# Performance work log

Hardware: AMD Instinct MI355X
Metric: run time of the kernel (lower is better)

## Reference

```python
import jax, jax.numpy as jnp
import numpy as np

E, D, H, K, N = 8, 512, 2048, 2, 1024  # experts, d_model, d_hidden, top_k, tokens
EPS = 1e-5


def _moe_linear(x, idx, W, b):
    # x: (M, in); idx: (M,) expert id per row; W: (E, out, in); b: (E, out)
    # Brute-force: compute per-expert dense GEMMs, select via one-hot (matches
    # BruteForceMoELinear math: y[i] = x[i] @ W[idx[i]].T + b[idx[i]]).
    m = jax.nn.one_hot(idx, W.shape[0], dtype=x.dtype)  # (M, E)
    y = jnp.einsum('me,eoi,mi->mo', m, W, x)
    return y + jnp.take(b, idx, axis=0)


def _forward(inp, gate_w, gate_b, w1, b1, w2, b2, ln_w, ln_b):
    # NaiveGate: linear -> top_k -> softmax over top-k logits
    logits = inp @ gate_w.T + gate_b              # (N, E)
    top_val, top_idx = jax.lax.top_k(logits, K)   # (N, K)
    score = jax.nn.softmax(top_val, axis=-1)      # (N, K)
    # repeat_interleave tokens, dispatch to experts
    x = jnp.repeat(inp, K, axis=0)                # (N*K, D)
    idx = top_idx.reshape(-1)                     # (N*K,)
    x = _moe_linear(x, idx, w1, b1)               # (N*K, H)
    x = jax.nn.gelu(x, approximate=False)         # torch F.gelu default = erf
    x = _moe_linear(x, idx, w2, b2)               # (N*K, D)
    x = x.reshape(N, K, D)
    x = jnp.einsum('nk,nkd->nd', score, x)        # bmm((N,1,K),(N,K,D)) combine
    # post layer norm (pre_lnorm=False)
    mu = jnp.mean(x, axis=-1, keepdims=True)
    var = jnp.var(x, axis=-1, keepdims=True)
    return (x - mu) * jax.lax.rsqrt(var + EPS) * ln_w + ln_b


def setup_inputs() -> dict:
    key = jax.random.key(0)
    ks = jax.random.split(key, 8)
    s = 0.02
    return {
        'inp': jax.random.normal(ks[0], (N, D), dtype=jnp.float32),
        'gate_w': s * jax.random.normal(ks[1], (E, D), dtype=jnp.float32),
        'gate_b': jnp.zeros((E,), dtype=jnp.float32),
        'w1': s * jax.random.normal(ks[2], (E, H, D), dtype=jnp.float32),
        'b1': jnp.zeros((E, H), dtype=jnp.float32),
        'w2': s * jax.random.normal(ks[3], (E, D, H), dtype=jnp.float32),
        'b2': jnp.zeros((E, D), dtype=jnp.float32),
        'ln_w': jnp.ones((D,), dtype=jnp.float32),
        'ln_b': jnp.zeros((D,), dtype=jnp.float32),
    }


def reference(inp, gate_w, gate_b, w1, b1, w2, b2, ln_w, ln_b):
    return _forward(inp, gate_w, gate_b, w1, b1, w2, b2, ln_w, ln_b)
```

## Files before the change

kernel.cpp:

```cpp
#include <hip/hip_runtime.h>
#include <cstdint>
#include <cstddef>

typedef _Float16 half_t;
typedef _Float16 half8 __attribute__((ext_vector_type(8)));
typedef float floatx4 __attribute__((ext_vector_type(4)));

#define E_ 8
#define D_ 512
#define H_ 2048
#define NTOK 1024
#define NP 2048
#define TM 64
#define MAX_TILES 40

__device__ __forceinline__ float gelu_f(float x) {
    return 0.5f * x * (1.0f + erff(x * 0.7071067811865476f));
}

__device__ __forceinline__ void gload_lds16(const half_t* g, half_t* l) {
    __builtin_amdgcn_global_load_lds(
        (__attribute__((address_space(1))) void*)(g),
        (__attribute__((address_space(3))) void*)(l),
        16, 0, 0);
}

__global__ __launch_bounds__(256) void gate_kernel(
        const float* __restrict__ inp, const float* __restrict__ gate_w,
        const float* __restrict__ gate_b, float* __restrict__ logits) {
    int n = blockIdx.x * 4 + (threadIdx.x >> 6);
    int lane = threadIdx.x & 63;
    const floatx4* xr = (const floatx4*)(inp + (size_t)n * D_);
    floatx4 x0 = xr[lane * 2], x1 = xr[lane * 2 + 1];
    #pragma unroll
    for (int e = 0; e < E_; e++) {
        const floatx4* gr = (const floatx4*)(gate_w + (size_t)e * D_);
        floatx4 g0 = gr[lane * 2], g1 = gr[lane * 2 + 1];
        float p = x0[0]*g0[0] + x0[1]*g0[1] + x0[2]*g0[2] + x0[3]*g0[3]
                + x1[0]*g1[0] + x1[1]*g1[1] + x1[2]*g1[2] + x1[3]*g1[3];
        #pragma unroll
        for (int m = 1; m < 64; m <<= 1) p += __shfl_xor(p, m);
        if (lane == 0) logits[(size_t)n * E_ + e] = p + gate_b[e];
    }
}

__global__ __launch_bounds__(256) void plan_kernel(
        const float* __restrict__ logits, float* __restrict__ score,
        int* __restrict__ idx, int* __restrict__ pos_of_pair,
        int* __restrict__ tile_e, int* __restrict__ tile_row0,
        int* __restrict__ tile_cnt, int* __restrict__ ntiles) {
    __shared__ int cnt_s[E_], off_s[E_ + 1], cur_s[E_];
    int tid = threadIdx.x;
    if (tid < E_) { cnt_s[tid] = 0; cur_s[tid] = 0; }
    __syncthreads();
    int my_e[4][2];
    #pragma unroll
    for (int i = 0; i < 4; i++) {
        int n = tid + i * 256;
        float l[E_];
        #pragma unroll
        for (int e = 0; e < E_; e++) l[e] = logits[(size_t)n * E_ + e];
        int e0 = 0; float v0 = l[0];
        #pragma unroll
        for (int e = 1; e < E_; e++) if (l[e] > v0) { v0 = l[e]; e0 = e; }
        int e1 = -1; float v1 = -3.4e38f;
        #pragma unroll
        for (int e = 0; e < E_; e++) if (e != e0 && l[e] > v1) { v1 = l[e]; e1 = e; }
        float s1 = expf(v1 - v0);
        float den = 1.0f + s1;
        score[2 * n]     = 1.0f / den;
        score[2 * n + 1] = s1 / den;
        idx[2 * n]     = e0;
        idx[2 * n + 1] = e1;
        atomicAdd(&cnt_s[e0], 1);
        atomicAdd(&cnt_s[e1], 1);
        my_e[i][0] = e0; my_e[i][1] = e1;
    }
    __syncthreads();
    if (tid == 0) {
        int o = 0;
        #pragma unroll
        for (int e = 0; e < E_; e++) { off_s[e] = o; o += cnt_s[e]; }
        off_s[E_] = o;
        int t = 0;
        for (int e = 0; e < E_; e++) {
            int c = cnt_s[e];
            int nt = (c + TM - 1) / TM;
            for (int i = 0; i < nt; i++) {
                tile_e[t] = e;
                tile_row0[t] = off_s[e] + i * TM;
                int rem = c - i * TM;
                tile_cnt[t] = rem < TM ? rem : TM;
                t++;
            }
        }
        ntiles[0] = t;
    }
    __syncthreads();
    #pragma unroll
    for (int i = 0; i < 4; i++) {
        #pragma unroll
        for (int k = 0; k < 2; k++) {
            int p = (tid + i * 256) * 2 + k;
            int e = my_e[i][k];
            int r = atomicAdd(&cur_s[e], 1);
            pos_of_pair[p] = off_s[e] + r;
        }
    }
}

__global__ __launch_bounds__(256) void scatter_kernel(
        const float* __restrict__ inp, const int* __restrict__ pos_of_pair,
        half_t* __restrict__ Xg) {
    int p = blockIdx.x * 4 + (threadIdx.x >> 6);
    int lane = threadIdx.x & 63;
    int pos = pos_of_pair[p];
    int n = p >> 1;
    const floatx4* src = (const floatx4*)(inp + (size_t)n * D_);
    floatx4 f0 = src[lane * 2], f1 = src[lane * 2 + 1];
    half8 h = { (half_t)f0[0], (half_t)f0[1], (half_t)f0[2], (half_t)f0[3],
                (half_t)f1[0], (half_t)f1[1], (half_t)f1[2], (half_t)f1[3] };
    *(half8*)(Xg + (size_t)pos * D_ + lane * 8) = h;
}

__global__ __launch_bounds__(256) void gemm1_kernel(
        const half_t* __restrict__ Xg, const float* __restrict__ w1,
        const float* __restrict__ b1,
        const int* __restrict__ tile_e, const int* __restrict__ tile_row0,
        const int* __restrict__ tile_cnt, const int* __restrict__ ntiles,
        half_t* __restrict__ Y1) {
    __shared__ half_t As[2][64 * 64];
    __shared__ half_t Bs[2][128 * 64];
    int t = blockIdx.x;
    if (t >= ntiles[0]) return;
    int e = tile_e[t], row0 = tile_row0[t], cnt = tile_cnt[t];
    int colbase = blockIdx.y * 128;
    int tid = threadIdx.x;
    int wave = tid >> 6, lane = tid & 63;
    int quad = lane >> 4, l16 = lane & 15;
    int wm = (wave & 1) * 32, wn = (wave >> 1) * 64;
    int xm = l16 & 7;

    int gr = tid >> 3, gc = tid & 7;
    int gsw = gc ^ (gr & 7);

    const half_t* Ag0 = Xg + (size_t)(row0 + gr) * D_ + gsw * 8;
    const half_t* Ag1 = Ag0 + 32 * D_;
    const float* Bg = w1 + ((size_t)e * H_ + colbase + gr) * D_ + gc * 8;
    int bslot = gr * 64 + gsw * 8;

    floatx4 br0[4], br1[4];

    #define STAGEA1(buf, k0) do { \
        gload_lds16(Ag0 + (k0), &As[buf][(size_t)tid * 8]); \
        gload_lds16(Ag1 + (k0), &As[buf][(size_t)(tid + 256) * 8]); } while (0)

    #define LOADB1(k0) do { \
        _Pragma("unroll") \
        for (int i = 0; i < 4; i++) { \
            const floatx4* p = (const floatx4*)(Bg + (size_t)i * 32 * D_ + (k0)); \
            br0[i] = p[0]; br1[i] = p[1]; } } while (0)

    #define CVTWRB1(buf) do { \
        _Pragma("unroll") \
        for (int i = 0; i < 4; i++) { \
            half8 h = { (half_t)br0[i][0], (half_t)br0[i][1], (half_t)br0[i][2], (half_t)br0[i][3], \
                        (half_t)br1[i][0], (half_t)br1[i][1], (half_t)br1[i][2], (half_t)br1[i][3] }; \
            *(half8*)(&Bs[buf][bslot + i * 2048]) = h; } } while (0)

    floatx4 acc[2][4] = {};
    STAGEA1(0, 0);
    LOADB1(0);
    CVTWRB1(0);
    __syncthreads();
    int cur = 0;
    for (int k0 = 0; k0 < D_; k0 += 64) {
        bool more = (k0 + 64) < D_;
        if (more) { STAGEA1(cur ^ 1, k0 + 64); LOADB1(k0 + 64); }
        const half_t* Ab = &As[cur][0];
        const half_t* Bb = &Bs[cur][0];
        #pragma unroll
        for (int ks = 0; ks < 2; ks++) {
            half8 a[2], b[4];
            #pragma unroll
            for (int mi = 0; mi < 2; mi++)
                a[mi] = *(const half8*)(Ab + (wm + mi * 16 + l16) * 64 + ((ks * 4 + quad) ^ xm) * 8);
            #pragma unroll
            for (int ni = 0; ni < 4; ni++)
                b[ni] = *(const half8*)(Bb + (wn + ni * 16 + l16) * 64 + ((ks * 4 + quad) ^ xm) * 8);
            #pragma unroll
            for (int mi = 0; mi < 2; mi++)
                #pragma unroll
                for (int ni = 0; ni < 4; ni++)
                    acc[mi][ni] = __builtin_amdgcn_mfma_f32_16x16x32_f16(a[mi], b[ni], acc[mi][ni], 0, 0, 0);
        }
        if (more) CVTWRB1(cur ^ 1);
        __syncthreads();
        cur ^= 1;
    }
    #undef STAGEA1
    #undef LOADB1
    #undef CVTWRB1

    float bias[4];
    #pragma unroll
    for (int ni = 0; ni < 4; ni++)
        bias[ni] = b1[(size_t)e * H_ + colbase + wn + ni * 16 + l16];
    #pragma unroll
    for (int mi = 0; mi < 2; mi++) {
        #pragma unroll
        for (int r = 0; r < 4; r++) {
            int rr = wm + mi * 16 + quad * 4 + r;
            if (rr >= cnt) continue;
            size_t rowoff = (size_t)(row0 + rr) * H_;
            #pragma unroll
            for (int ni = 0; ni < 4; ni++) {
                float v = acc[mi][ni][r] + bias[ni];
                Y1[rowoff + colbase + wn + ni * 16 + l16] = (half_t)gelu_f(v);
            }
        }
    }
}

__global__ __launch_bounds__(256) void gemm2_kernel(
        const half_t* __restrict__ Y1, const float* __restrict__ w2,
        const int* __restrict__ tile_e, const int* __restrict__ tile_row0,
        const int* __restrict__ tile_cnt, const int* __restrict__ ntiles,
        float* __restrict__ Y2p) {
    __shared__ half_t As[2][64 * 64];
    __shared__ half_t Bs[2][128 * 64];
    int t = blockIdx.x;
    if (t >= ntiles[0]) return;
    int e = tile_e[t], row0 = tile_row0[t], cnt = tile_cnt[t];
    int colbase = blockIdx.y * 128;
    int kz = blockIdx.z;
    int kzbase = kz * 512;
    int tid = threadIdx.x;
    int wave = tid >> 6, lane = tid & 63;
    int quad = lane >> 4, l16 = lane & 15;
    int wm = (wave & 1) * 32, wn = (wave >> 1) * 64;
    int xm = l16 & 7;

    int gr = tid >> 3, gc = tid & 7;
    int gsw = gc ^ (gr & 7);

    const half_t* Ag0 = Y1 + (size_t)(row0 + gr) * H_ + kzbase + gsw * 8;
    const half_t* Ag1 = Ag0 + 32 * H_;
    const float* Bg = w2 + ((size_t)e * D_ + colbase + gr) * H_ + kzbase + gc * 8;
    int bslot = gr * 64 + gsw * 8;

    floatx4 br0[4], br1[4];

    #define STAGEA2(buf, k0) do { \
        gload_lds16(Ag0 + (k0), &As[buf][(size_t)tid * 8]); \
        gload_lds16(Ag1 + (k0), &As[buf][(size_t)(tid + 256) * 8]); } while (0)

    #define LOADB2(k0) do { \
        _Pragma("unroll") \
        for (int i = 0; i < 4; i++) { \
            const floatx4* p = (const floatx4*)(Bg + (size_t)i * 32 * H_ + (k0)); \
            br0[i] = p[0]; br1[i] = p[1]; } } while (0)

    #define CVTWRB2(buf) do { \
        _Pragma("unroll") \
        for (int i = 0; i < 4; i++) { \
            half8 h = { (half_t)br0[i][0], (half_t)br0[i][1], (half_t)br0[i][2], (half_t)br0[i][3], \
                        (half_t)br1[i][0], (half_t)br1[i][1], (half_t)br1[i][2], (half_t)br1[i][3] }; \
            *(half8*)(&Bs[buf][bslot + i * 2048]) = h; } } while (0)

    floatx4 acc[2][4] = {};
    STAGEA2(0, 0);
    LOADB2(0);
    CVTWRB2(0);
    __syncthreads();
    int cur = 0;
    for (int k0 = 0; k0 < 512; k0 += 64) {
        bool more = (k0 + 64) < 512;
        if (more) { STAGEA2(cur ^ 1, k0 + 64); LOADB2(k0 + 64); }
        const half_t* Ab = &As[cur][0];
        const half_t* Bb = &Bs[cur][0];
        #pragma unroll
        for (int ks = 0; ks < 2; ks++) {
            half8 a[2], b[4];
            #pragma unroll
            for (int mi = 0; mi < 2; mi++)
                a[mi] = *(const half8*)(Ab + (wm + mi * 16 + l16) * 64 + ((ks * 4 + quad) ^ xm) * 8);
            #pragma unroll
            for (int ni = 0; ni < 4; ni++)
                b[ni] = *(const half8*)(Bb + (wn + ni * 16 + l16) * 64 + ((ks * 4 + quad) ^ xm) * 8);
            #pragma unroll
            for (int mi = 0; mi < 2; mi++)
                #pragma unroll
                for (int ni = 0; ni < 4; ni++)
                    acc[mi][ni] = __builtin_amdgcn_mfma_f32_16x16x32_f16(a[mi], b[ni], acc[mi][ni], 0, 0, 0);
        }
        if (more) CVTWRB2(cur ^ 1);
        __syncthreads();
        cur ^= 1;
    }
    #undef STAGEA2
    #undef LOADB2
    #undef CVTWRB2

    #pragma unroll
    for (int mi = 0; mi < 2; mi++) {
        #pragma unroll
        for (int r = 0; r < 4; r++) {
            int rr = wm + mi * 16 + quad * 4 + r;
            if (rr >= cnt) continue;
            size_t rowoff = ((size_t)kz * NP + row0 + rr) * D_;
            #pragma unroll
            for (int ni = 0; ni < 4; ni++)
                Y2p[rowoff + colbase + wn + ni * 16 + l16] = acc[mi][ni][r];
        }
    }
}

__global__ __launch_bounds__(256) void final_kernel(
        const float* __restrict__ Y2p, const float* __restrict__ b2,
        const int* __restrict__ idx, const float* __restrict__ score,
        const int* __restrict__ pos_of_pair,
        const float* __restrict__ ln_w, const float* __restrict__ ln_b,
        float* __restrict__ out) {
    int n = blockIdx.x * 4 + (threadIdx.x >> 6);
    int lane = threadIdx.x & 63;
    int p0 = pos_of_pair[2 * n], p1 = pos_of_pair[2 * n + 1];
    int e0 = idx[2 * n], e1 = idx[2 * n + 1];
    float s0 = score[2 * n], s1 = score[2 * n + 1];

    const floatx4* b2r0 = (const floatx4*)(b2 + (size_t)e0 * D_);
    const floatx4* b2r1 = (const floatx4*)(b2 + (size_t)e1 * D_);
    floatx4 a_lo = b2r0[lane * 2], a_hi = b2r0[lane * 2 + 1];
    floatx4 c_lo = b2r1[lane * 2], c_hi = b2r1[lane * 2 + 1];
    #pragma unroll
    for (int kz = 0; kz < 4; kz++) {
        const floatx4* r0 = (const floatx4*)(Y2p + ((size_t)kz * NP + p0) * D_);
        const floatx4* r1 = (const floatx4*)(Y2p + ((size_t)kz * NP + p1) * D_);
        a_lo += r0[lane * 2]; a_hi += r0[lane * 2 + 1];
        c_lo += r1[lane * 2]; c_hi += r1[lane * 2 + 1];
    }
    floatx4 y_lo = s0 * a_lo + s1 * c_lo;
    floatx4 y_hi = s0 * a_hi + s1 * c_hi;

    float s = 0.0f, q = 0.0f;
    #pragma unroll
    for (int j = 0; j < 4; j++) {
        s += y_lo[j] + y_hi[j];
        q += y_lo[j] * y_lo[j] + y_hi[j] * y_hi[j];
    }
    #pragma unroll
    for (int m = 1; m < 64; m <<= 1) {
        s += __shfl_xor(s, m);
        q += __shfl_xor(q, m);
    }
    float mean = s * (1.0f / 512.0f);
    float var = q * (1.0f / 512.0f) - mean * mean;
    float inv = 1.0f / sqrtf(var + 1e-5f);

    const floatx4* wv = (const floatx4*)ln_w;
    const floatx4* bv = (const floatx4*)ln_b;
    floatx4 o_lo = (y_lo - mean) * inv * wv[lane * 2]     + bv[lane * 2];
    floatx4 o_hi = (y_hi - mean) * inv * wv[lane * 2 + 1] + bv[lane * 2 + 1];
    floatx4* op = (floatx4*)(out + (size_t)n * D_);
    op[lane * 2] = o_lo;
    op[lane * 2 + 1] = o_hi;
}

extern "C" void kernel_launch(void* const* d_in, const int* in_sizes, int n_in,
                              void* d_out, int out_size, void* d_ws, size_t ws_size,
                              hipStream_t stream) {
    const float* inp    = (const float*)d_in[0];
    const float* gate_w = (const float*)d_in[1];
    const float* gate_b = (const float*)d_in[2];
    const float* w1     = (const float*)d_in[3];
    const float* b1     = (const float*)d_in[4];
    const float* w2     = (const float*)d_in[5];
    const float* b2     = (const float*)d_in[6];
    const float* ln_w   = (const float*)d_in[7];
    const float* ln_b   = (const float*)d_in[8];
    float* out = (float*)d_out;

    char* ws = (char*)d_ws;
    size_t o = 0;
    auto carve = [&](size_t bytes) -> char* {
        char* p = ws + o;
        o += (bytes + 255) & ~(size_t)255;
        return p;
    };
    half_t* Xg  = (half_t*)carve(sizeof(half_t) * (size_t)(NP + 128) * D_);
    half_t* Y1  = (half_t*)carve(sizeof(half_t) * (size_t)(NP + 128) * H_);
    float*  Y2p = (float*)carve(sizeof(float) * 4 * (size_t)NP * D_);
    float*  logits = (float*)carve(sizeof(float) * NTOK * E_);
    float*  score  = (float*)carve(sizeof(float) * NP);
    int* idx         = (int*)carve(sizeof(int) * NP);
    int* pos_of_pair = (int*)carve(sizeof(int) * NP);
    int* tile_e      = (int*)carve(sizeof(int) * MAX_TILES);
    int* tile_row0   = (int*)carve(sizeof(int) * MAX_TILES);
    int* tile_cnt    = (int*)carve(sizeof(int) * MAX_TILES);
    int* ntiles      = (int*)carve(sizeof(int) * 1);

    gate_kernel<<<NTOK / 4, 256, 0, stream>>>(inp, gate_w, gate_b, logits);
    plan_kernel<<<1, 256, 0, stream>>>(logits, score, idx, pos_of_pair,
                                       tile_e, tile_row0, tile_cnt, ntiles);
    scatter_kernel<<<NP / 4, 256, 0, stream>>>(inp, pos_of_pair, Xg);
    gemm1_kernel<<<dim3(MAX_TILES, H_ / 128), 256, 0, stream>>>(
        Xg, w1, b1, tile_e, tile_row0, tile_cnt, ntiles, Y1);
    gemm2_kernel<<<dim3(MAX_TILES, D_ / 128, 4), 256, 0, stream>>>(
        Y1, w2, tile_e, tile_row0, tile_cnt, ntiles, Y2p);
    final_kernel<<<NTOK / 4, 256, 0, stream>>>(Y2p, b2, idx, score, pos_of_pair, ln_w, ln_b, out);
}
```

Measured before the change: 178.0 us.

## Fuse token gather into GEMM1, shrink N-tiles to 64, remap blocks across XCDs

```diff
diff --git a/kernel.cpp b/kernel.cpp
--- a/kernel.cpp
+++ b/kernel.cpp
@@ -18,11 +18,10 @@
     return 0.5f * x * (1.0f + erff(x * 0.7071067811865476f));
 }
 
-__device__ __forceinline__ void gload_lds16(const half_t* g, half_t* l) {
-    __builtin_amdgcn_global_load_lds(
-        (__attribute__((address_space(1))) void*)(g),
-        (__attribute__((address_space(3))) void*)(l),
-        16, 0, 0);
+__device__ __forceinline__ half8 cvt8(floatx4 a, floatx4 b) {
+    half8 h = { (half_t)a[0], (half_t)a[1], (half_t)a[2], (half_t)a[3],
+                (half_t)b[0], (half_t)b[1], (half_t)b[2], (half_t)b[3] };
+    return h;
 }
 
 __global__ __launch_bounds__(256) void gate_kernel(
@@ -47,6 +46,7 @@
 __global__ __launch_bounds__(256) void plan_kernel(
         const float* __restrict__ logits, float* __restrict__ score,
         int* __restrict__ idx, int* __restrict__ pos_of_pair,
+        int* __restrict__ tok_of_pos,
         int* __restrict__ tile_e, int* __restrict__ tile_row0,
         int* __restrict__ tile_cnt, int* __restrict__ ntiles) {
     __shared__ int cnt_s[E_], off_s[E_ + 1], cur_s[E_];
@@ -104,107 +104,94 @@
             int p = (tid + i * 256) * 2 + k;
             int e = my_e[i][k];
             int r = atomicAdd(&cur_s[e], 1);
-            pos_of_pair[p] = off_s[e] + r;
-        }
-    }
-}
-
-__global__ __launch_bounds__(256) void scatter_kernel(
-        const float* __restrict__ inp, const int* __restrict__ pos_of_pair,
-        half_t* __restrict__ Xg) {
-    int p = blockIdx.x * 4 + (threadIdx.x >> 6);
-    int lane = threadIdx.x & 63;
-    int pos = pos_of_pair[p];
-    int n = p >> 1;
-    const floatx4* src = (const floatx4*)(inp + (size_t)n * D_);
-    floatx4 f0 = src[lane * 2], f1 = src[lane * 2 + 1];
-    half8 h = { (half_t)f0[0], (half_t)f0[1], (half_t)f0[2], (half_t)f0[3],
-                (half_t)f1[0], (half_t)f1[1], (half_t)f1[2], (half_t)f1[3] };
-    *(half8*)(Xg + (size_t)pos * D_ + lane * 8) = h;
+            int pos = off_s[e] + r;
+            pos_of_pair[p] = pos;
+            tok_of_pos[pos] = p >> 1;
+        }
+    }
 }
 
 __global__ __launch_bounds__(256) void gemm1_kernel(
-        const half_t* __restrict__ Xg, const float* __restrict__ w1,
-        const float* __restrict__ b1,
+        const float* __restrict__ inp, const int* __restrict__ tok_of_pos,
+        const float* __restrict__ w1, const float* __restrict__ b1,
         const int* __restrict__ tile_e, const int* __restrict__ tile_row0,
         const int* __restrict__ tile_cnt, const int* __restrict__ ntiles,
         half_t* __restrict__ Y1) {
     __shared__ half_t As[2][64 * 64];
-    __shared__ half_t Bs[2][128 * 64];
-    int t = blockIdx.x;
+    __shared__ half_t Bs[2][64 * 64];
+    int flat = blockIdx.x + gridDim.x * blockIdx.y;
+    int per = (gridDim.x * gridDim.y) >> 3;
+    int f2 = (flat & 7) * per + (flat >> 3);
+    int t = f2 % MAX_TILES;
+    int cb = f2 / MAX_TILES;
     if (t >= ntiles[0]) return;
     int e = tile_e[t], row0 = tile_row0[t], cnt = tile_cnt[t];
-    int colbase = blockIdx.y * 128;
+    int colbase = cb * 64;
     int tid = threadIdx.x;
     int wave = tid >> 6, lane = tid & 63;
     int quad = lane >> 4, l16 = lane & 15;
-    int wm = (wave & 1) * 32, wn = (wave >> 1) * 64;
+    int wm = (wave & 1) * 32, wn = (wave >> 1) * 32;
     int xm = l16 & 7;
 
-    int gr = tid >> 3, gc = tid & 7;
-    int gsw = gc ^ (gr & 7);
-
-    const half_t* Ag0 = Xg + (size_t)(row0 + gr) * D_ + gsw * 8;
-    const half_t* Ag1 = Ag0 + 32 * D_;
-    const float* Bg = w1 + ((size_t)e * H_ + colbase + gr) * D_ + gc * 8;
-    int bslot = gr * 64 + gsw * 8;
-
-    floatx4 br0[4], br1[4];
-
-    #define STAGEA1(buf, k0) do { \
-        gload_lds16(Ag0 + (k0), &As[buf][(size_t)tid * 8]); \
-        gload_lds16(Ag1 + (k0), &As[buf][(size_t)(tid + 256) * 8]); } while (0)
-
-    #define LOADB1(k0) do { \
-        _Pragma("unroll") \
-        for (int i = 0; i < 4; i++) { \
-            const floatx4* p = (const floatx4*)(Bg + (size_t)i * 32 * D_ + (k0)); \
-            br0[i] = p[0]; br1[i] = p[1]; } } while (0)
-
-    #define CVTWRB1(buf) do { \
-        _Pragma("unroll") \
-        for (int i = 0; i < 4; i++) { \
-            half8 h = { (half_t)br0[i][0], (half_t)br0[i][1], (half_t)br0[i][2], (half_t)br0[i][3], \
-                        (half_t)br1[i][0], (half_t)br1[i][1], (half_t)br1[i][2], (half_t)br1[i][3] }; \
-            *(half8*)(&Bs[buf][bslot + i * 2048]) = h; } } while (0)
-
-    floatx4 acc[2][4] = {};
-    STAGEA1(0, 0);
-    LOADB1(0);
-    CVTWRB1(0);
+    int gr0 = tid >> 3, gr1 = gr0 + 32, gc = tid & 7;
+    int sw0 = gc ^ (gr0 & 7), sw1 = gc ^ (gr1 & 7);
+    int ar0 = row0 + gr0; if (ar0 > NP - 1) ar0 = NP - 1;
+    int ar1 = row0 + gr1; if (ar1 > NP - 1) ar1 = NP - 1;
+    int tok0 = tok_of_pos[ar0];
+    int tok1 = tok_of_pos[ar1];
+    const floatx4* Ag0 = (const floatx4*)(inp + (size_t)tok0 * D_) + gc * 2;
+    const floatx4* Ag1 = (const floatx4*)(inp + (size_t)tok1 * D_) + gc * 2;
+    const floatx4* Bg0 = (const floatx4*)(w1 + ((size_t)e * H_ + colbase + gr0) * D_) + gc * 2;
+    const floatx4* Bg1 = (const floatx4*)(w1 + ((size_t)e * H_ + colbase + gr1) * D_) + gc * 2;
+    int sa0 = gr0 * 64 + sw0 * 8, sa1 = gr1 * 64 + sw1 * 8;
+
+    floatx4 ra0a, ra0b, ra1a, ra1b, rb0a, rb0b, rb1a, rb1b;
+    #define LOAD1(kq) do { \
+        ra0a = Ag0[kq]; ra0b = Ag0[(kq) + 1]; \
+        ra1a = Ag1[kq]; ra1b = Ag1[(kq) + 1]; \
+        rb0a = Bg0[kq]; rb0b = Bg0[(kq) + 1]; \
+        rb1a = Bg1[kq]; rb1b = Bg1[(kq) + 1]; } while (0)
+    #define CVW1(buf) do { \
+        *(half8*)(&As[buf][sa0]) = cvt8(ra0a, ra0b); \
+        *(half8*)(&As[buf][sa1]) = cvt8(ra1a, ra1b); \
+        *(half8*)(&Bs[buf][sa0]) = cvt8(rb0a, rb0b); \
+        *(half8*)(&Bs[buf][sa1]) = cvt8(rb1a, rb1b); } while (0)
+
+    floatx4 acc[2][2] = {};
+    LOAD1(0);
+    CVW1(0);
     __syncthreads();
     int cur = 0;
     for (int k0 = 0; k0 < D_; k0 += 64) {
         bool more = (k0 + 64) < D_;
-        if (more) { STAGEA1(cur ^ 1, k0 + 64); LOADB1(k0 + 64); }
+        if (more) LOAD1((k0 + 64) >> 2);
         const half_t* Ab = &As[cur][0];
         const half_t* Bb = &Bs[cur][0];
         #pragma unroll
         for (int ks = 0; ks < 2; ks++) {
-            half8 a[2], b[4];
+            half8 a[2], b[2];
             #pragma unroll
             for (int mi = 0; mi < 2; mi++)
                 a[mi] = *(const half8*)(Ab + (wm + mi * 16 + l16) * 64 + ((ks * 4 + quad) ^ xm) * 8);
             #pragma unroll
-            for (int ni = 0; ni < 4; ni++)
+            for (int ni = 0; ni < 2; ni++)
                 b[ni] = *(const half8*)(Bb + (wn + ni * 16 + l16) * 64 + ((ks * 4 + quad) ^ xm) * 8);
             #pragma unroll
             for (int mi = 0; mi < 2; mi++)
                 #pragma unroll
-                for (int ni = 0; ni < 4; ni++)
+                for (int ni = 0; ni < 2; ni++)
                     acc[mi][ni] = __builtin_amdgcn_mfma_f32_16x16x32_f16(a[mi], b[ni], acc[mi][ni], 0, 0, 0);
         }
-        if (more) CVTWRB1(cur ^ 1);
+        if (more) CVW1(cur ^ 1);
         __syncthreads();
         cur ^= 1;
     }
-    #undef STAGEA1
-    #undef LOADB1
-    #undef CVTWRB1
-
-    float bias[4];
-    #pragma unroll
-    for (int ni = 0; ni < 4; ni++)
+    #undef LOAD1
+    #undef CVW1
+
+    float bias[2];
+    #pragma unroll
+    for (int ni = 0; ni < 2; ni++)
         bias[ni] = b1[(size_t)e * H_ + colbase + wn + ni * 16 + l16];
     #pragma unroll
     for (int mi = 0; mi < 2; mi++) {
@@ -214,7 +201,7 @@
             if (rr >= cnt) continue;
             size_t rowoff = (size_t)(row0 + rr) * H_;
             #pragma unroll
-            for (int ni = 0; ni < 4; ni++) {
+            for (int ni = 0; ni < 2; ni++) {
                 float v = acc[mi][ni][r] + bias[ni];
                 Y1[rowoff + colbase + wn + ni * 16 + l16] = (half_t)gelu_f(v);
             }
@@ -228,79 +215,75 @@
         const int* __restrict__ tile_cnt, const int* __restrict__ ntiles,
         float* __restrict__ Y2p) {
     __shared__ half_t As[2][64 * 64];
-    __shared__ half_t Bs[2][128 * 64];
-    int t = blockIdx.x;
+    __shared__ half_t Bs[2][64 * 64];
+    int flat = blockIdx.x + gridDim.x * (blockIdx.y + gridDim.y * blockIdx.z);
+    int per = (gridDim.x * gridDim.y * gridDim.z) >> 3;
+    int f2 = (flat & 7) * per + (flat >> 3);
+    int t = f2 % MAX_TILES;
+    int rest = f2 / MAX_TILES;
+    int cb = rest & 7;
+    int kz = rest >> 3;
     if (t >= ntiles[0]) return;
     int e = tile_e[t], row0 = tile_row0[t], cnt = tile_cnt[t];
-    int colbase = blockIdx.y * 128;
-    int kz = blockIdx.z;
+    int colbase = cb * 64;
     int kzbase = kz * 512;
     int tid = threadIdx.x;
     int wave = tid >> 6, lane = tid & 63;
     int quad = lane >> 4, l16 = lane & 15;
-    int wm = (wave & 1) * 32, wn = (wave >> 1) * 64;
+    int wm = (wave & 1) * 32, wn = (wave >> 1) * 32;
     int xm = l16 & 7;
 
-    int gr = tid >> 3, gc = tid & 7;
-    int gsw = gc ^ (gr & 7);
-
-    const half_t* Ag0 = Y1 + (size_t)(row0 + gr) * H_ + kzbase + gsw * 8;
-    const half_t* Ag1 = Ag0 + 32 * H_;
-    const float* Bg = w2 + ((size_t)e * D_ + colbase + gr) * H_ + kzbase + gc * 8;
-    int bslot = gr * 64 + gsw * 8;
-
-    floatx4 br0[4], br1[4];
-
-    #define STAGEA2(buf, k0) do { \
-        gload_lds16(Ag0 + (k0), &As[buf][(size_t)tid * 8]); \
-        gload_lds16(Ag1 + (k0), &As[buf][(size_t)(tid + 256) * 8]); } while (0)
-
-    #define LOADB2(k0) do { \
-        _Pragma("unroll") \
-        for (int i = 0; i < 4; i++) { \
-            const floatx4* p = (const floatx4*)(Bg + (size_t)i * 32 * H_ + (k0)); \
-            br0[i] = p[0]; br1[i] = p[1]; } } while (0)
-
-    #define CVTWRB2(buf) do { \
-        _Pragma("unroll") \
-        for (int i = 0; i < 4; i++) { \
-            half8 h = { (half_t)br0[i][0], (half_t)br0[i][1], (half_t)br0[i][2], (half_t)br0[i][3], \
-                        (half_t)br1[i][0], (half_t)br1[i][1], (half_t)br1[i][2], (half_t)br1[i][3] }; \
-            *(half8*)(&Bs[buf][bslot + i * 2048]) = h; } } while (0)
-
-    floatx4 acc[2][4] = {};
-    STAGEA2(0, 0);
-    LOADB2(0);
-    CVTWRB2(0);
+    int gr0 = tid >> 3, gr1 = gr0 + 32, gc = tid & 7;
+    int sw0 = gc ^ (gr0 & 7), sw1 = gc ^ (gr1 & 7);
+    const half8* Ag0 = (const half8*)(Y1 + (size_t)(row0 + gr0) * H_ + kzbase) + gc;
+    const half8* Ag1 = (const half8*)(Y1 + (size_t)(row0 + gr1) * H_ + kzbase) + gc;
+    const floatx4* Bg0 = (const floatx4*)(w2 + ((size_t)e * D_ + colbase + gr0) * H_ + kzbase) + gc * 2;
+    const floatx4* Bg1 = (const floatx4*)(w2 + ((size_t)e * D_ + colbase + gr1) * H_ + kzbase) + gc * 2;
+    int sa0 = gr0 * 64 + sw0 * 8, sa1 = gr1 * 64 + sw1 * 8;
+
+    half8 ha0, ha1;
+    floatx4 rb0a, rb0b, rb1a, rb1b;
+    #define LOAD2(k0) do { \
+        ha0 = Ag0[(k0) >> 3]; ha1 = Ag1[(k0) >> 3]; \
+        rb0a = Bg0[(k0) >> 2]; rb0b = Bg0[((k0) >> 2) + 1]; \
+        rb1a = Bg1[(k0) >> 2]; rb1b = Bg1[((k0) >> 2) + 1]; } while (0)
+    #define CVW2(buf) do { \
+        *(half8*)(&As[buf][sa0]) = ha0; \
+        *(half8*)(&As[buf][sa1]) = ha1; \
+        *(half8*)(&Bs[buf][sa0]) = cvt8(rb0a, rb0b); \
+        *(half8*)(&Bs[buf][sa1]) = cvt8(rb1a, rb1b); } while (0)
+
+    floatx4 acc[2][2] = {};
+    LOAD2(0);
+    CVW2(0);
     __syncthreads();
     int cur = 0;
     for (int k0 = 0; k0 < 512; k0 += 64) {
         bool more = (k0 + 64) < 512;
-        if (more) { STAGEA2(cur ^ 1, k0 + 64); LOADB2(k0 + 64); }
+        if (more) LOAD2(k0 + 64);
         const half_t* Ab = &As[cur][0];
         const half_t* Bb = &Bs[cur][0];
         #pragma unroll
         for (int ks = 0; ks < 2; ks++) {
-            half8 a[2], b[4];
+            half8 a[2], b[2];
             #pragma unroll
             for (int mi = 0; mi < 2; mi++)
                 a[mi] = *(const half8*)(Ab + (wm + mi * 16 + l16) * 64 + ((ks * 4 + quad) ^ xm) * 8);
             #pragma unroll
-            for (int ni = 0; ni < 4; ni++)
+            for (int ni = 0; ni < 2; ni++)
                 b[ni] = *(const half8*)(Bb + (wn + ni * 16 + l16) * 64 + ((ks * 4 + quad) ^ xm) * 8);
             #pragma unroll
             for (int mi = 0; mi < 2; mi++)
                 #pragma unroll
-                for (int ni = 0; ni < 4; ni++)
+                for (int ni = 0; ni < 2; ni++)
                     acc[mi][ni] = __builtin_amdgcn_mfma_f32_16x16x32_f16(a[mi], b[ni], acc[mi][ni], 0, 0, 0);
         }
-        if (more) CVTWRB2(cur ^ 1);
+        if (more) CVW2(cur ^ 1);
         __syncthreads();
         cur ^= 1;
     }
-    #undef STAGEA2
-    #undef LOADB2
-    #undef CVTWRB2
+    #undef LOAD2
+    #undef CVW2
 
     #pragma unroll
     for (int mi = 0; mi < 2; mi++) {
@@ -310,7 +293,7 @@
             if (rr >= cnt) continue;
             size_t rowoff = ((size_t)kz * NP + row0 + rr) * D_;
             #pragma unroll
-            for (int ni = 0; ni < 4; ni++)
+            for (int ni = 0; ni < 2; ni++)
                 Y2p[rowoff + colbase + wn + ni * 16 + l16] = acc[mi][ni][r];
         }
     }
@@ -387,25 +370,24 @@
         o += (bytes + 255) & ~(size_t)255;
         return p;
     };
-    half_t* Xg  = (half_t*)carve(sizeof(half_t) * (size_t)(NP + 128) * D_);
     half_t* Y1  = (half_t*)carve(sizeof(half_t) * (size_t)(NP + 128) * H_);
     float*  Y2p = (float*)carve(sizeof(float) * 4 * (size_t)NP * D_);
     float*  logits = (float*)carve(sizeof(float) * NTOK * E_);
     float*  score  = (float*)carve(sizeof(float) * NP);
     int* idx         = (int*)carve(sizeof(int) * NP);
     int* pos_of_pair = (int*)carve(sizeof(int) * NP);
+    int* tok_of_pos  = (int*)carve(sizeof(int) * NP);
     int* tile_e      = (int*)carve(sizeof(int) * MAX_TILES);
     int* tile_row0   = (int*)carve(sizeof(int) * MAX_TILES);
     int* tile_cnt    = (int*)carve(sizeof(int) * MAX_TILES);
     int* ntiles      = (int*)carve(sizeof(int) * 1);
 
     gate_kernel<<<NTOK / 4, 256, 0, stream>>>(inp, gate_w, gate_b, logits);
-    plan_kernel<<<1, 256, 0, stream>>>(logits, score, idx, pos_of_pair,
+    plan_kernel<<<1, 256, 0, stream>>>(logits, score, idx, pos_of_pair, tok_of_pos,
                                        tile_e, tile_row0, tile_cnt, ntiles);
-    scatter_kernel<<<NP / 4, 256, 0, stream>>>(inp, pos_of_pair, Xg);
-    gemm1_kernel<<<dim3(MAX_TILES, H_ / 128), 256, 0, stream>>>(
-        Xg, w1, b1, tile_e, tile_row0, tile_cnt, ntiles, Y1);
-    gemm2_kernel<<<dim3(MAX_TILES, D_ / 128, 4), 256, 0, stream>>>(
+    gemm1_kernel<<<dim3(MAX_TILES, H_ / 64), 256, 0, stream>>>(
+        inp, tok_of_pos, w1, b1, tile_e, tile_row0, tile_cnt, ntiles, Y1);
+    gemm2_kernel<<<dim3(MAX_TILES, D_ / 64, 4), 256, 0, stream>>>(
         Y1, w2, tile_e, tile_row0, tile_cnt, ntiles, Y2p);
     final_kernel<<<NTOK / 4, 256, 0, stream>>>(Y2p, b2, idx, score, pos_of_pair, ln_w, ln_b, out);
 }
```

Result: faster. 169.5 us (-4.8%).
